# Performance work log

Measured on AMD Instinct MI355X. Metric: run time of the kernel, lower is better.

Reference implementation:

```python
import jax, jax.numpy as jnp
import numpy as np

K_UPPER = 196608  # number of smallest-|grad| positions to mask per sample


def setup_inputs() -> dict:
    key = jax.random.key(0)
    k1, k2 = jax.random.split(key)
    x = jax.random.normal(k1, (64, 3, 512, 512), dtype=jnp.float32)
    grad = jax.random.normal(k2, (64, 3, 512, 512), dtype=jnp.float32)
    return {"x": x, "grad": grad}


def _mask_low_gradient(x, grad):
    # x, grad: [B, C, H, W]
    B, C, H, W = x.shape
    hw = H * W
    flat_g = grad.reshape(B, -1)                                  # [B, C*H*W]
    # _sort: k smallest absolute gradients -> top_k of negated abs (unsorted ok)
    _neg_vals, idx = jax.lax.top_k(-jnp.abs(flat_g), K_UPPER)     # idx: [B, K]
    # channel containing each selected flat index (matches the torch range test)
    ch = idx // hw                                                # [B, K]
    xc = x.reshape(B, C, hw)
    # Faithful to source: torch slice [start:channel_indexes] EXCLUDES the last
    # element of each channel when computing min/max.
    mn = jnp.min(xc[:, :, : hw - 1], axis=-1)                     # [B, C]
    mx = jnp.max(xc[:, :, : hw - 1], axis=-1)                     # [B, C]
    lo = jnp.take_along_axis(mn, ch, axis=1)                      # [B, K]
    hi = jnp.take_along_axis(mx, ch, axis=1)                      # [B, K]
    # uniform fill in [lo, hi) per masked element
    u = jax.random.uniform(jax.random.key(42), idx.shape, dtype=x.dtype)
    fill = lo + u * (hi - lo)                                     # [B, K]
    flat_x = x.reshape(B, -1)
    out = flat_x.at[jnp.arange(B)[:, None], idx].set(fill)
    return out.reshape(x.shape)


def reference(x, grad):
    return _mask_low_gradient(x, grad)
```

## Files before the change

### kernel.cpp

```cpp
#include <hip/hip_runtime.h>
#include <stdint.h>

#define TPB 256
#define TPS 1024

constexpr int BN   = 64;
constexpr int CCH  = 3;
constexpr int HWS  = 262144;
constexpr int LOG_HW = 18;
constexpr int NPS  = 786432;
constexpr int KSEL = 196608;
constexpr int KCAP = 200704;
constexpr int NB_T = 32;
constexpr int CH_T = NPS / NB_T;
constexpr int NB_C = 64;
constexpr int CH_C = NPS / NB_C;
constexpr int NRNG = 768;
constexpr int NB_S = 8;
constexpr int CH_S = KCAP / NB_S;
constexpr int TILE = 4096;
constexpr int NBINS = 2048;
constexpr int SUB  = 8;
constexpr int NFB  = 49;
constexpr int ASLOT = 256;
constexpr int ACAP = NRNG * ASLOT;
constexpr int BMPW = NPS / 32;

typedef unsigned u32x4 __attribute__((ext_vector_type(4)));

constexpr int WS_MN   = 0;
constexpr int WS_MX   = 192;
constexpr int WS_V1   = 384;
constexpr int WS_B1   = 448;
constexpr int WS_V2   = 512;
constexpr int WS_GS   = 576;
constexpr int WS_KP   = 640;
constexpr int WS_S0   = 704;
constexpr int WS_S01  = 768;
constexpr int WS_CNT  = 832;
constexpr int WS_COFF = WS_CNT + BN * NRNG;
constexpr int WS_MNP  = WS_COFF + BN * NRNG;
constexpr int WS_MXP  = WS_MNP + BN * CCH * SUB;
constexpr int WS_CNT2 = WS_MXP + BN * CCH * SUB;
constexpr int WS_RC   = WS_CNT2 + BN * NRNG;
constexpr int WS_CHC  = WS_RC + BN * NRNG;
constexpr int WS_THA  = WS_CHC + BN * 4;
constexpr int WS_THB  = WS_THA + BN * NBINS;
constexpr int WS_H0   = WS_THB + BN * NBINS;
constexpr int WS_H1   = WS_H0 + BN * 256 * NB_S;
constexpr int WS_H2   = WS_H1 + BN * 256 * NB_S;
constexpr int WS_H3   = WS_H2 + BN * 256 * NB_S;
constexpr int WS_HF   = WS_H3 + BN * 256 * NB_S;
constexpr size_t WS_FIX_END = (size_t)WS_HF + (size_t)BN * 64 * NB_S;
constexpr size_t RECW = (size_t)BN * KCAP * 2;
constexpr size_t WS_NEEDED_BYTES = (WS_FIX_END + 2 * RECW) * 4;
constexpr size_t WS_BMP_OFF = WS_FIX_END + 2 * RECW;
constexpr size_t WS_NEEDED_BMP = (WS_BMP_OFF + (size_t)BN * BMPW) * 4;
static_assert((size_t)BN * ACAP <= RECW, "append scratch must fit in R2");

__device__ __forceinline__ unsigned rotl32(unsigned x, int r) { return (x << r) | (x >> (32 - r)); }

__device__ __forceinline__ void tf4(unsigned& x0, unsigned& x1, int a, int b, int c, int d) {
  x0 += x1; x1 = rotl32(x1, a); x1 ^= x0;
  x0 += x1; x1 = rotl32(x1, b); x1 ^= x0;
  x0 += x1; x1 = rotl32(x1, c); x1 ^= x0;
  x0 += x1; x1 = rotl32(x1, d); x1 ^= x0;
}

__device__ __forceinline__ void threefry2x32(unsigned k0, unsigned k1, unsigned c0, unsigned c1,
                                             unsigned& o0, unsigned& o1) {
  const unsigned ks2 = k0 ^ k1 ^ 0x1BD11BDAu;
  unsigned x0 = c0 + k0, x1 = c1 + k1;
  tf4(x0, x1, 13, 15, 26, 6);  x0 += k1;  x1 += ks2 + 1u;
  tf4(x0, x1, 17, 29, 16, 24); x0 += ks2; x1 += k0 + 2u;
  tf4(x0, x1, 13, 15, 26, 6);  x0 += k0;  x1 += k1 + 3u;
  tf4(x0, x1, 17, 29, 16, 24); x0 += k1;  x1 += ks2 + 4u;
  tf4(x0, x1, 13, 15, 26, 6);  x0 += ks2; x1 += k0 + 5u;
  o0 = x0; o1 = x1;
}

__global__ __launch_bounds__(TPB) void k_zero(unsigned* __restrict__ p, int n) {
  int i = blockIdx.x * TPB + threadIdx.x;
  if (i < n) p[i] = 0u;
}

__global__ __launch_bounds__(TPB) void k_mnmx(const float4* __restrict__ x,
                                              unsigned* __restrict__ ws) {
  __shared__ float smn[TPB], smx[TPB];
  const int g = blockIdx.x;
  const int bc = g / SUB, sub = g - bc * SUB;
  const int Q4 = HWS / 4 / SUB;
  const size_t base4 = (size_t)bc * (HWS / 4) + (size_t)sub * Q4;
  const bool last = (sub == SUB - 1);
  const int tid = threadIdx.x;
  float lo = 3.4e38f, hi = -3.4e38f;
  for (int i = tid; i < Q4; i += TPB) {
    float4 v = x[base4 + i];
    if (last && i == Q4 - 1) {
      lo = fminf(lo, fminf(fminf(v.x, v.y), v.z));
      hi = fmaxf(hi, fmaxf(fmaxf(v.x, v.y), v.z));
    } else {
      lo = fminf(lo, fminf(fminf(v.x, v.y), fminf(v.z, v.w)));
      hi = fmaxf(hi, fmaxf(fmaxf(v.x, v.y), fmaxf(v.z, v.w)));
    }
  }
  smn[tid] = lo; smx[tid] = hi; __syncthreads();
  for (int s = TPB / 2; s > 0; s >>= 1) {
    if (tid < s) { smn[tid] = fminf(smn[tid], smn[tid + s]); smx[tid] = fmaxf(smx[tid], smx[tid + s]); }
    __syncthreads();
  }
  if (tid == 0) {
    ((float*)(ws + WS_MNP))[g] = smn[0];
    ((float*)(ws + WS_MXP))[g] = smx[0];
  }
}

__global__ __launch_bounds__(TPB) void k_mnfin(unsigned* __restrict__ ws) {
  const int t = threadIdx.x;
  if (t < BN * CCH) {
    const float* mnp = (const float*)(ws + WS_MNP);
    const float* mxp = (const float*)(ws + WS_MXP);
    float lo = 3.4e38f, hi = -3.4e38f;
    for (int s = 0; s < SUB; ++s) {
      lo = fminf(lo, mnp[t * SUB + s]);
      hi = fmaxf(hi, mxp[t * SUB + s]);
    }
    ((float*)(ws + WS_MN))[t] = lo;
    ((float*)(ws + WS_MX))[t] = hi;
  }
}

__global__ __launch_bounds__(TPB) void k_thrA(const unsigned* __restrict__ gb, unsigned* __restrict__ hist) {
  __shared__ unsigned h[NBINS];
  const int b = blockIdx.y, blk = blockIdx.x, tid = threadIdx.x;
  for (int v = tid; v < NBINS; v += TPB) h[v] = 0u;
  __syncthreads();
  const uint4* g4 = (const uint4*)(gb + (size_t)b * NPS + (size_t)blk * CH_T);
  for (int i = tid; i < CH_T / 4; i += TPB) {
    uint4 v = g4[i];
    atomicAdd(&h[(v.x & 0x7FFFFFFFu) >> 21], 1u);
    atomicAdd(&h[(v.y & 0x7FFFFFFFu) >> 21], 1u);
    atomicAdd(&h[(v.z & 0x7FFFFFFFu) >> 21], 1u);
    atomicAdd(&h[(v.w & 0x7FFFFFFFu) >> 21], 1u);
  }
  __syncthreads();
  unsigned* gh = hist + (size_t)b * NBINS;
  for (int v = tid; v < NBINS; v += TPB) if (h[v]) atomicAdd(&gh[v], h[v]);
}

__global__ __launch_bounds__(TPB) void k_thrBC(const unsigned* __restrict__ gb,
                                               unsigned* __restrict__ hist,
                                               unsigned* __restrict__ app,
                                               unsigned* __restrict__ ws) {
  __shared__ unsigned h[NBINS];
  __shared__ unsigned chs[3];
  const int bid = blockIdx.x;
  const int b = bid & 63, blk = bid >> 6, tid = threadIdx.x;
  const int lane = tid & 63, wv = tid >> 6;
  const unsigned long long ltm = (1ull << lane) - 1ull;
  for (int v = tid; v < NBINS; v += TPB) h[v] = 0u;
  if (tid < 3) chs[tid] = 0u;
  __syncthreads();
  const unsigned V1 = ws[WS_V1 + b];
  const uint4* g4 = (const uint4*)(gb + (size_t)b * NPS + (size_t)blk * CH_C) + wv * 768;
  unsigned cc0 = 0, cc1 = 0, cc2 = 0;
  for (int r = 0; r < 3; ++r) {
    const unsigned rangeId = (unsigned)((blk * 4 + wv) * 3 + r);
    unsigned* ap = app + (size_t)b * ACAP + (size_t)rangeId * ASLOT;
    unsigned abase = 0, cntLess = 0;
#pragma unroll
    for (int it = 0; it < 4; ++it) {
      const uint4 v = g4[r * 256 + it * 64 + lane];
      const unsigned e = (unsigned)blk * CH_C + (unsigned)wv * 3072u + (unsigned)r * 1024u
                       + (unsigned)it * 256u + (unsigned)lane * 4u;
      const unsigned k[4] = { v.x & 0x7FFFFFFFu, v.y & 0x7FFFFFFFu, v.z & 0x7FFFFFFFu, v.w & 0x7FFFFFFFu };
#pragma unroll
      for (int c = 0; c < 4; ++c) {
        const unsigned top = k[c] >> 21;
        const bool isEq = (top == V1);
        if (top < V1) {
          ++cntLess;
          const unsigned ch = (e + (unsigned)c) >> LOG_HW;
          if (ch == 0) ++cc0; else if (ch == 1) ++cc1; else ++cc2;
        } else if (isEq) {
          atomicAdd(&h[(k[c] >> 10) & 2047u], 1u);
        }
        unsigned long long m = __ballot(isEq);
        if (isEq) {
          const unsigned ai = abase + (unsigned)__popcll(m & ltm);
          if (ai < (unsigned)ASLOT) {
            const unsigned ch = (e + (unsigned)c) >> LOG_HW;
            ap[ai] = (ch << 11) | ((k[c] >> 10) & 2047u);
          }
        }
        abase += (unsigned)__popcll(m);
      }
    }
    unsigned cl = cntLess;
    for (int off = 32; off >= 1; off >>= 1) cl += __shfl_down(cl, off, 64);
    if (lane == 0) {
      ws[WS_CNT + b * NRNG + rangeId] = cl;
      ws[WS_RC + b * NRNG + rangeId] = min(abase, (unsigned)ASLOT);
    }
  }
  if (cc0) atomicAdd(&chs[0], cc0);
  if (cc1) atomicAdd(&chs[1], cc1);
  if (cc2) atomicAdd(&chs[2], cc2);
  __syncthreads();
  if (tid < 3 && chs[tid]) atomicAdd(&ws[WS_CHC + b * 4 + tid], chs[tid]);
  unsigned* gh = hist + (size_t)b * NBINS;
  for (int v = tid; v < NBINS; v += TPB) if (h[v]) atomicAdd(&gh[v], h[v]);
}

__global__ __launch_bounds__(TPB) void k_find(const unsigned* __restrict__ hist,
                                              unsigned* __restrict__ ws, int mode) {
  __shared__ unsigned part[TPB];
  const int b = blockIdx.x, tid = threadIdx.x;
  const unsigned* h = hist + (size_t)b * NBINS;
  const int per = NBINS / TPB;
  const unsigned Kt = (mode == 0) ? (unsigned)KSEL : (unsigned)KSEL - ws[WS_B1 + b];
  unsigned vals[8];
  unsigned s = 0;
  for (int j = 0; j < per; ++j) { vals[j] = h[tid * per + j]; s += vals[j]; }
  part[tid] = s; __syncthreads();
  for (int off = 1; off < TPB; off <<= 1) {
    unsigned t = (tid >= off) ? part[tid - off] : 0u;
    __syncthreads(); part[tid] += t; __syncthreads();
  }
  unsigned run = part[tid] - s;
  for (int j = 0; j < per; ++j) {
    const unsigned lo = run, c = vals[j];
    run += c;
    if (lo < Kt && Kt <= run) {
      const unsigned v = (unsigned)(tid * per + j);
      if (mode == 0) {
        ws[WS_V1 + b] = v; ws[WS_B1 + b] = lo;
      } else {
        ws[WS_V2 + b] = v;
        const unsigned T22 = (ws[WS_V1 + b] << 11) | v;
        ws[WS_GS + b] = (T22 << 10) | 1023u;
        unsigned kp = ws[WS_B1 + b] + lo + c;
        if (kp > (unsigned)KCAP) kp = (unsigned)KCAP;
        ws[WS_KP + b] = kp;
      }
    }
  }
}

__global__ __launch_bounds__(TPB) void k_cc2(const unsigned* __restrict__ app,
                                             unsigned* __restrict__ ws) {
  __shared__ unsigned lch[3];
  const int b = blockIdx.x, tid = threadIdx.x;
  if (tid < 3) lch[tid] = 0u;
  __syncthreads();
  const unsigned V2 = ws[WS_V2 + b];
  unsigned c0 = 0, c1 = 0, c2 = 0;
  for (int j = 0; j < 3; ++j) {
    const int r = j * 256 + tid;
    const unsigned cnt = ws[WS_RC + b * NRNG + r];
    const unsigned* ap = app + (size_t)b * ACAP + (size_t)r * ASLOT;
    unsigned n2 = 0;
    for (unsigned i = 0; i < cnt; ++i) {
      const unsigned e = ap[i];
      if ((e & 2047u) <= V2) {
        ++n2;
        const unsigned ch = (e >> 11) & 3u;
        if (ch == 0) ++c0; else if (ch == 1) ++c1; else ++c2;
      }
    }
    ws[WS_CNT2 + b * NRNG + r] = n2;
  }
  if (c0) atomicAdd(&lch[0], c0);
  if (c1) atomicAdd(&lch[1], c1);
  if (c2) atomicAdd(&lch[2], c2);
  __syncthreads();
  if (tid < 3 && lch[tid]) atomicAdd(&ws[WS_CHC + b * 4 + tid], lch[tid]);
}

__global__ __launch_bounds__(TPB) void k_cscan(unsigned* __restrict__ ws) {
  __shared__ unsigned wsum[4];
  const int b = blockIdx.x, tid = threadIdx.x;
  const int lane = tid & 63, wv = tid >> 6;
  const unsigned c0 = ws[WS_CNT + b * NRNG + 3 * tid + 0] + ws[WS_CNT2 + b * NRNG + 3 * tid + 0];
  const unsigned c1 = ws[WS_CNT + b * NRNG + 3 * tid + 1] + ws[WS_CNT2 + b * NRNG + 3 * tid + 1];
  const unsigned c2 = ws[WS_CNT + b * NRNG + 3 * tid + 2] + ws[WS_CNT2 + b * NRNG + 3 * tid + 2];
  const unsigned s = c0 + c1 + c2;
  unsigned incl = s;
  for (int off = 1; off < 64; off <<= 1) {
    unsigned t = __shfl_up(incl, off, 64);
    if (lane >= off) incl += t;
  }
  if (lane == 63) wsum[wv] = incl;
  __syncthreads();
  unsigned wpre = 0;
  for (int w = 0; w < wv; ++w) wpre += wsum[w];
  const unsigned excl = incl - s + wpre;
  ws[WS_COFF + b * NRNG + 3 * tid + 0] = excl;
  ws[WS_COFF + b * NRNG + 3 * tid + 1] = excl + c0;
  ws[WS_COFF + b * NRNG + 3 * tid + 2] = excl + c0 + c1;
  if (tid == 0) {
    const unsigned s0 = ws[WS_CHC + b * 4 + 0];
    ws[WS_S0 + b] = s0;
    ws[WS_S01 + b] = s0 + ws[WS_CHC + b * 4 + 1];
  }
}

template<int BMP>
__global__ __launch_bounds__(TPB) void k_cscatter(const unsigned* __restrict__ gb,
                                                  const unsigned* __restrict__ ws,
                                                  unsigned* __restrict__ keyArr,
                                                  unsigned* __restrict__ H0,
                                                  unsigned* __restrict__ bmp) {
  __shared__ unsigned h2[256 * NB_S];
  const int bid = blockIdx.x;
  const int b = bid & 63, blk = bid >> 6, tid = threadIdx.x;
  const int lane = tid & 63, wv = tid >> 6;
  for (int e = tid; e < 256 * NB_S; e += TPB) h2[e] = 0u;
  __syncthreads();
  const unsigned G = ws[WS_GS + b];
  const uint4* g4 = (const uint4*)(gb + (size_t)b * NPS + (size_t)blk * CH_C) + wv * 768;
  unsigned* ka = keyArr + (size_t)b * KCAP;
  unsigned* bw = BMP ? (bmp + (size_t)b * BMPW + (size_t)blk * 384 + (size_t)wv * 96) : nullptr;
  for (int r = 0; r < 3; ++r) {
    unsigned base = ws[WS_COFF + b * NRNG + (blk * 4 + wv) * 3 + r];
#pragma unroll
    for (int it = 0; it < 4; ++it) {
      const uint4 v = g4[r * 256 + it * 64 + lane];
      unsigned k[4] = { v.x & 0x7FFFFFFFu, v.y & 0x7FFFFFFFu, v.z & 0x7FFFFFFFu, v.w & 0x7FFFFFFFu };
      unsigned nib = 0;
      unsigned cnt = 0;
      bool s[4];
#pragma unroll
      for (int c = 0; c < 4; ++c) {
        s[c] = (k[c] <= G);
        nib |= ((unsigned)s[c]) << c;
        cnt += (unsigned)s[c];
      }
      if (BMP) {
        unsigned w = nib << ((lane & 7) * 4);
        w |= __shfl_xor(w, 1, 64);
        w |= __shfl_xor(w, 2, 64);
        w |= __shfl_xor(w, 4, 64);
        if ((lane & 7) == 0) bw[r * 32 + it * 8 + (lane >> 3)] = w;
      }
      unsigned incl = cnt;
      for (int off = 1; off < 64; off <<= 1) {
        unsigned u = __shfl_up(incl, off, 64);
        if (lane >= off) incl += u;
      }
      const unsigned wtot = __shfl(incl, 63, 64);
      unsigned pos = base + incl - cnt;
#pragma unroll
      for (int c = 0; c < 4; ++c) {
        if (s[c]) {
          if (pos < (unsigned)KCAP) {
            ka[pos] = k[c];
            atomicAdd(&h2[(k[c] & 255u) * NB_S + pos / (unsigned)CH_S], 1u);
          }
          ++pos;
        }
      }
      base += wtot;
    }
  }
  __syncthreads();
  unsigned* Hb = H0 + (size_t)b * 256 * NB_S;
  for (int e = tid; e < 256 * NB_S; e += TPB) {
    unsigned c = h2[e];
    if (c) atomicAdd(&Hb[e], c);
  }
}

__global__ __launch_bounds__(TPB) void k_hscan(unsigned* __restrict__ H) {
  __shared__ unsigned wsum[4];
  const int b = blockIdx.x, tid = threadIdx.x;
  const int lane = tid & 63, wv = tid >> 6;
  unsigned* Hb = H + (size_t)b * 256 * NB_S;
  unsigned row[NB_S];
  unsigned run = 0;
#pragma unroll
  for (int k = 0; k < NB_S; ++k) {
    unsigned t = Hb[tid * NB_S + k];
    row[k] = run; run += t;
  }
  unsigned incl = run;
  for (int off = 1; off < 64; off <<= 1) {
    unsigned t = __shfl_up(incl, off, 64);
    if (lane >= off) incl += t;
  }
  if (lane == 63) wsum[wv] = incl;
  __syncthreads();
  unsigned wpre = 0;
  for (int w = 0; w < wv; ++w) wpre += wsum[w];
  const unsigned excl = incl - run + wpre;
#pragma unroll
  for (int k = 0; k < NB_S; ++k) Hb[tid * NB_S + k] = row[k] + excl;
}

__global__ __launch_bounds__(64) void k_hscanF(unsigned* __restrict__ Hf) {
  const int b = blockIdx.x, tid = threadIdx.x;
  unsigned* Hb = Hf + (size_t)b * 64 * NB_S;
  unsigned row[NB_S];
  unsigned run = 0;
  if (tid < NFB) {
#pragma unroll
    for (int k = 0; k < NB_S; ++k) {
      unsigned t = Hb[tid * NB_S + k];
      row[k] = run; run += t;
    }
  }
  unsigned incl = run;
  for (int off = 1; off < 64; off <<= 1) {
    unsigned t = __shfl_up(incl, off, 64);
    if (tid >= off) incl += t;
  }
  const unsigned excl = incl - run;
  if (tid < NFB) {
#pragma unroll
    for (int k = 0; k < NB_S; ++k) Hb[tid * NB_S + k] = row[k] + excl;
  }
}

template<int MODE>
__global__ __launch_bounds__(TPS) void k_sort8(const unsigned* __restrict__ keyIn,
                                               const uint2* __restrict__ inR,
                                               uint2* __restrict__ outR,
                                               const unsigned* __restrict__ Hcur,
                                               unsigned* __restrict__ Hnext,
                                               unsigned* __restrict__ Hf,
                                               const unsigned* __restrict__ ws,
                                               int shift) {
  __shared__ unsigned wh[16][256];
  __shared__ unsigned gout[256];
  __shared__ unsigned gbase[256];
  __shared__ unsigned wsum[4];
  __shared__ uint2    stg[TILE];
  __shared__ unsigned h2[256 * NB_S];
  __shared__ unsigned h2f[(MODE == 1) ? NFB * NB_S : 1];
  const int bid = blockIdx.x;
  const int b = bid & 63, blk = bid >> 6, tid = threadIdx.x;
  const int lane = tid & 63, wv = tid >> 6;
  const unsigned long long ltm = (1ull << lane) - 1ull;
  const unsigned kp = min(ws[WS_KP + b], (unsigned)KCAP);
  const unsigned s0 = (unsigned)blk * CH_S;
  const unsigned s1 = min(s0 + (unsigned)CH_S, kp);
  const unsigned* ki = keyIn + (size_t)b * KCAP;
  const uint2* in = inR + (size_t)b * KCAP;
  uint2* out = outR + (size_t)b * KCAP;
  const bool doF = (MODE == 1) && (Hf != nullptr);

  for (int d = tid; d < 256; d += TPS) gbase[d] = Hcur[((size_t)b * 256 + d) * NB_S + blk];
  for (int e = tid; e < 256 * NB_S; e += TPS) h2[e] = 0u;
  if (MODE == 1) { if (doF) for (int e = tid; e < NFB * NB_S; e += TPS) h2f[e] = 0u; }
  __syncthreads();

  for (unsigned t0 = s0; t0 < s1; t0 += (unsigned)TILE) {
    { uint4* w4 = (uint4*)&wh[0][0];
      w4[tid] = make_uint4(0u, 0u, 0u, 0u); }
    __syncthreads();

    unsigned key[4], cpp[4], wloc[4], dig[4];
    bool val[4];
    const unsigned wbase = t0 + (unsigned)wv * 256u;
#pragma unroll
    for (int c = 0; c < 4; ++c) {
      const unsigned i = wbase + (unsigned)c * 64u + (unsigned)lane;
      val[c] = (i < s1);
      if (MODE == 0) { cpp[c] = i; key[c] = val[c] ? ki[i] : 0u; }
      else { uint2 r = val[c] ? in[i] : make_uint2(0u, 0u); cpp[c] = r.x; key[c] = r.y; }
      dig[c] = (key[c] >> shift) & 255u;
      unsigned long long peers = __ballot(val[c]);
#pragma unroll
      for (int bit = 0; bit < 8; ++bit) {
        unsigned long long bb = __ballot(val[c] && ((dig[c] >> bit) & 1u));
        peers &= ((dig[c] >> bit) & 1u) ? bb : ~bb;
      }
      const unsigned before = (unsigned)__popcll(peers & ltm);
      int ldr = __ffsll((unsigned long long)peers) - 1;
      if (ldr < 0) ldr = 0;
      unsigned old = 0;
      if (val[c] && lane == ldr) old = atomicAdd(&wh[wv][dig[c]], (unsigned)__popcll(peers));
      old = __shfl(old, ldr, 64);
      wloc[c] = old + before;
    }
    __syncthreads();

    unsigned incl = 0, tot = 0;
    if (tid < 256) {
      const unsigned d = (unsigned)tid;
#pragma unroll
      for (int w = 0; w < 16; ++w) tot += wh[w][d];
      incl = tot;
      for (int off = 1; off < 64; off <<= 1) {
        unsigned t = __shfl_up(incl, off, 64);
        if (lane >= off) incl += t;
      }
      if (lane == 63) wsum[wv] = incl;
    }
    __syncthreads();
    if (tid < 256) {
      const unsigned d = (unsigned)tid;
      unsigned wpre = 0;
      for (int w = 0; w < wv; ++w) wpre += wsum[w];
      const unsigned tstart = incl - tot + wpre;
      const unsigned g = gbase[d];
      gout[d] = g - tstart;
      gbase[d] = g + tot;
      unsigned run = tstart;
#pragma unroll
      for (int w = 0; w < 16; ++w) { const unsigned t = wh[w][d]; wh[w][d] = run; run += t; }
    }
    __syncthreads();

#pragma unroll
    for (int c = 0; c < 4; ++c) {
      if (val[c]) {
        uint2 r; r.x = cpp[c]; r.y = key[c];
        stg[wh[wv][dig[c]] + wloc[c]] = r;
      }
    }
    __syncthreads();
    const unsigned nt = min((unsigned)TILE, s1 - t0);
    for (unsigned j = tid; j < nt; j += TPS) {
      const uint2 r = stg[j];
      const unsigned d = (r.y >> shift) & 255u;
      const unsigned pos = gout[d] + j;
      out[pos] = r;
      const unsigned nd = (r.y >> (shift + 8)) & 255u;
      atomicAdd(&h2[nd * NB_S + pos / (unsigned)CH_S], 1u);
      if (doF) atomicAdd(&h2f[(r.x >> 12) * NB_S + pos / (unsigned)CH_S], 1u);
    }
    __syncthreads();
  }

  {
    unsigned* Hb = Hnext + (size_t)b * 256 * NB_S;
    for (int e = tid; e < 256 * NB_S; e += TPS) {
      unsigned c = h2[e];
      if (c) atomicAdd(&Hb[e], c);
    }
    if (doF) {
      unsigned* Hfb = Hf + (size_t)b * 64 * NB_S;
      for (int e = tid; e < NFB * NB_S; e += TPS) {
        unsigned c = h2f[e];
        if (c) atomicAdd(&Hfb[e], c);
      }
    }
  }
}

__global__ __launch_bounds__(TPS) void k_final(const uint2* __restrict__ inR,
                                               uint2* __restrict__ pairOut,
                                               const unsigned* __restrict__ Hcur,
                                               const unsigned* __restrict__ Hf,
                                               const unsigned* __restrict__ ws) {
  __shared__ unsigned wh[16][128];
  __shared__ unsigned gbase[128];
  __shared__ unsigned whF[16][64];
  __shared__ unsigned goutF[64];
  __shared__ unsigned gbaseF[64];
  __shared__ uint2    stg[TILE];
  const int bid = blockIdx.x;
  const int b = bid & 63, blk = bid >> 6, tid = threadIdx.x;
  const int lane = tid & 63, wv = tid >> 6;
  const unsigned long long ltm = (1ull << lane) - 1ull;
  const unsigned kp = min(ws[WS_KP + b], (unsigned)KCAP);
  const unsigned s0 = (unsigned)blk * CH_S;
  const unsigned s1 = min(s0 + (unsigned)CH_S, kp);
  const uint2* in = inR + (size_t)b * KCAP;
  uint2* po = pairOut + (size_t)b * KCAP;

  for (int d = tid; d < 128; d += TPS) gbase[d] = Hcur[((size_t)b * 256 + d) * NB_S + blk];
  for (int d = tid; d < 64; d += TPS)
    gbaseF[d] = (d < NFB) ? Hf[((size_t)b * 64 + d) * NB_S + blk] : 0u;
  __syncthreads();

  for (unsigned t0 = s0; t0 < s1; t0 += (unsigned)TILE) {
    { uint4* p = (uint4*)&wh[0][0];
      if (tid < 512) p[tid] = make_uint4(0u, 0u, 0u, 0u);
      uint4* q = (uint4*)&whF[0][0];
      if (tid >= 512 && tid < 768) q[tid - 512] = make_uint4(0u, 0u, 0u, 0u); }
    __syncthreads();

    unsigned key[4], cpp[4], wloc[4], dig[4];
    bool val[4];
    const unsigned wbase = t0 + (unsigned)wv * 256u;
#pragma unroll
    for (int c = 0; c < 4; ++c) {
      const unsigned i = wbase + (unsigned)c * 64u + (unsigned)lane;
      val[c] = (i < s1);
      uint2 r = val[c] ? in[i] : make_uint2(0u, 0u);
      cpp[c] = r.x; key[c] = r.y;
      dig[c] = (key[c] >> 24) & 127u;
      unsigned long long peers = __ballot(val[c]);
#pragma unroll
      for (int bit = 0; bit < 7; ++bit) {
        unsigned long long bb = __ballot(val[c] && ((dig[c] >> bit) & 1u));
        peers &= ((dig[c] >> bit) & 1u) ? bb : ~bb;
      }
      const unsigned before = (unsigned)__popcll(peers & ltm);
      int ldr = __ffsll((unsigned long long)peers) - 1;
      if (ldr < 0) ldr = 0;
      unsigned old = 0;
      if (val[c] && lane == ldr) old = atomicAdd(&wh[wv][dig[c]], (unsigned)__popcll(peers));
      old = __shfl(old, ldr, 64);
      wloc[c] = old + before;
    }
    __syncthreads();

    if (tid < 128) {
      const unsigned d = (unsigned)tid;
      unsigned run = gbase[d];
#pragma unroll
      for (int w = 0; w < 16; ++w) { const unsigned t = wh[w][d]; wh[w][d] = run; run += t; }
      gbase[d] = run;
    }
    __syncthreads();

    unsigned rnk[4], dbF[4], wlocF[4];
#pragma unroll
    for (int c = 0; c < 4; ++c) {
      dbF[c] = cpp[c] >> 12;
      if (val[c]) {
        rnk[c] = wh[wv][dig[c]] + wloc[c];
        wlocF[c] = atomicAdd(&whF[wv][dbF[c]], 1u);
      }
    }
    __syncthreads();

    if (tid < 64) {
      const unsigned d = (unsigned)tid;
      unsigned tot = 0;
      if (d < NFB) {
#pragma unroll
        for (int w = 0; w < 16; ++w) tot += whF[w][d];
      }
      unsigned incl = tot;
      for (int off = 1; off < 64; off <<= 1) {
        unsigned t = __shfl_up(incl, off, 64);
        if (lane >= off) incl += t;
      }
      const unsigned tstart = incl - tot;
      goutF[d] = gbaseF[d] - tstart;
      gbaseF[d] += tot;
      unsigned run = tstart;
#pragma unroll
      for (int w = 0; w < 16; ++w) { const unsigned t = whF[w][d]; whF[w][d] = run; run += t; }
    }
    __syncthreads();

#pragma unroll
    for (int c = 0; c < 4; ++c) {
      if (val[c]) {
        uint2 r; r.x = cpp[c]; r.y = rnk[c];
        stg[whF[wv][dbF[c]] + wlocF[c]] = r;
      }
    }
    __syncthreads();

    const unsigned nt = min((unsigned)TILE, s1 - t0);
    for (unsigned j = tid; j < nt; j += TPS) {
      const uint2 r = stg[j];
      po[goutF[r.x >> 12] + j] = r;
    }
    __syncthreads();
  }
}

__global__ __launch_bounds__(TPB) void k_unpack(const uint2* __restrict__ pairs,
                                                unsigned* __restrict__ fm,
                                                const unsigned* __restrict__ ws) {
  __shared__ unsigned vals[4096];
  const int bid = blockIdx.x;
  const int b = bid & 63, d = bid >> 6, tid = threadIdx.x;
  const unsigned kp = min(ws[WS_KP + b], (unsigned)KCAP);
  const unsigned start = (unsigned)d * 4096u;
  if (start >= kp) return;
  const unsigned cnt = min(4096u, kp - start);
  const unsigned S0 = ws[WS_S0 + b], S01 = ws[WS_S01 + b];
  const float* mnf = (const float*)(ws + WS_MN);
  const float* mxf = (const float*)(ws + WS_MX);
  const float l0 = mnf[b * CCH], l1 = mnf[b * CCH + 1], l2 = mnf[b * CCH + 2];
  const float h0 = mxf[b * CCH], h1 = mxf[b * CCH + 1], h2v = mxf[b * CCH + 2];
  const uint2* pb = pairs + (size_t)b * KCAP + start;
  for (unsigned j = tid; j < cnt; j += TPB) {
    const uint2 r = pb[j];
    unsigned res = 0xFFFFFFFFu;
    if (r.y < (unsigned)KSEL) {
      const unsigned p = (unsigned)b * (unsigned)KSEL + r.y;
      unsigned o0, o1;
      threefry2x32(0u, 42u, 0u, p, o0, o1);
      const unsigned bits = o0 ^ o1;
      const float u = __uint_as_float((bits >> 9) | 0x3f800000u) - 1.0f;
      const unsigned ch = (unsigned)(r.x >= S0) + (unsigned)(r.x >= S01);
      const float lo = (ch == 0) ? l0 : ((ch == 1) ? l1 : l2);
      const float hi = (ch == 0) ? h0 : ((ch == 1) ? h1 : h2v);
      res = __float_as_uint(lo + u * (hi - lo));
    }
    vals[r.x & 4095u] = res;
  }
  __syncthreads();
  unsigned* f = fm + (size_t)b * KCAP + start;
  for (unsigned j = tid; j < cnt; j += TPB) f[j] = vals[j];
}

template<int BMP>
__global__ __launch_bounds__(TPB) void k_fill(const u32x4* __restrict__ x4,
                                              const u32x4* __restrict__ g4all,
                                              const unsigned* __restrict__ bmp,
                                              const unsigned* __restrict__ fillmap,
                                              const unsigned* __restrict__ ws,
                                              u32x4* __restrict__ out4) {
  const int bid = blockIdx.x;
  const int b = bid & 63, blk = bid >> 6, tid = threadIdx.x;
  const int lane = tid & 63, wv = tid >> 6;
  const unsigned G = ws[WS_GS + b];
  const unsigned kp = min(ws[WS_KP + b], (unsigned)KCAP);
  const size_t t4 = (size_t)b * (NPS / 4) + (size_t)blk * (CH_C / 4) + (size_t)wv * 768;
  const unsigned* fm = fillmap + (size_t)b * KCAP;
  const unsigned* bw = BMP ? (bmp + (size_t)b * BMPW + (size_t)blk * 384 + (size_t)wv * 96) : nullptr;
  for (int r = 0; r < 3; ++r) {
    unsigned base = ws[WS_COFF + b * NRNG + (blk * 4 + wv) * 3 + r];
#pragma unroll
    for (int it = 0; it < 4; ++it) {
      const size_t a = t4 + r * 256 + it * 64 + lane;
      u32x4 xv = __builtin_nontemporal_load(&x4[a]);
      unsigned nib;
      if (BMP) {
        const unsigned w = bw[r * 32 + it * 8 + (lane >> 3)];
        nib = (w >> ((lane & 7) * 4)) & 0xFu;
      } else {
        const u32x4 gv = __builtin_nontemporal_load(&g4all[a]);
        nib = (unsigned)((gv.x & 0x7FFFFFFFu) <= G)
            | ((unsigned)((gv.y & 0x7FFFFFFFu) <= G) << 1)
            | ((unsigned)((gv.z & 0x7FFFFFFFu) <= G) << 2)
            | ((unsigned)((gv.w & 0x7FFFFFFFu) <= G) << 3);
      }
      const unsigned cnt = (unsigned)__popc(nib);
      unsigned incl = cnt;
      for (int off = 1; off < 64; off <<= 1) {
        unsigned u = __shfl_up(incl, off, 64);
        if (lane >= off) incl += u;
      }
      const unsigned wtot = __shfl(incl, 63, 64);
      unsigned pos = base + incl - cnt;
#pragma unroll
      for (int c = 0; c < 4; ++c) {
        if ((nib >> c) & 1u) {
          if (pos < kp) {
            const unsigned rr = fm[pos];
            if (rr != 0xFFFFFFFFu) xv[c] = rr;
          }
          ++pos;
        }
      }
      __builtin_nontemporal_store(xv, &out4[a]);
      base += wtot;
    }
  }
}

extern "C" void kernel_launch(void* const* d_in, const int* in_sizes, int n_in,
                              void* d_out, int out_size, void* d_ws, size_t ws_size,
                              hipStream_t stream) {
  const float* x = (const float*)d_in[0];
  const unsigned* gb = (const unsigned*)d_in[1];
  float* out = (float*)d_out;
  unsigned* ws = (unsigned*)d_ws;
  if (ws_size < WS_NEEDED_BYTES) return;
  const bool useBmp = (ws_size >= WS_NEEDED_BMP);

  unsigned* R1 = ws + WS_FIX_END;
  unsigned* R2 = ws + WS_FIX_END + RECW;
  unsigned* BMP = ws + WS_BMP_OFF;
  unsigned* H0 = ws + WS_H0;
  unsigned* H1 = ws + WS_H1;
  unsigned* H2 = ws + WS_H2;
  unsigned* H3 = ws + WS_H3;
  unsigned* HF = ws + WS_HF;

  dim3 blk(TPB);
  dim3 sblk(TPS);

  k_mnmx<<<dim3(BN * CCH * SUB), blk, 0, stream>>>((const float4*)x, ws);
  k_mnfin<<<dim3(1), blk, 0, stream>>>(ws);
  {
    const int nz = (int)(WS_FIX_END - WS_CHC);
    k_zero<<<dim3((nz + TPB - 1) / TPB), blk, 0, stream>>>(ws + WS_CHC, nz);
  }

  k_thrA<<<dim3(NB_T, BN), blk, 0, stream>>>(gb, ws + WS_THA);
  k_find<<<dim3(BN), blk, 0, stream>>>(ws + WS_THA, ws, 0);
  k_thrBC<<<dim3(NB_C * BN), blk, 0, stream>>>(gb, ws + WS_THB, R2, ws);
  k_find<<<dim3(BN), blk, 0, stream>>>(ws + WS_THB, ws, 1);
  k_cc2<<<dim3(BN), blk, 0, stream>>>(R2, ws);
  k_cscan<<<dim3(BN), blk, 0, stream>>>(ws);

  if (useBmp) k_cscatter<1><<<dim3(NB_C * BN), blk, 0, stream>>>(gb, ws, R1, H0, BMP);
  else        k_cscatter<0><<<dim3(NB_C * BN), blk, 0, stream>>>(gb, ws, R1, H0, nullptr);

  k_hscan<<<dim3(BN), blk, 0, stream>>>(H0);
  k_sort8<0><<<dim3(NB_S * BN), sblk, 0, stream>>>(R1, (const uint2*)nullptr, (uint2*)R2, H0, H1, nullptr, ws, 0);
  k_hscan<<<dim3(BN), blk, 0, stream>>>(H1);
  k_sort8<1><<<dim3(NB_S * BN), sblk, 0, stream>>>(nullptr, (const uint2*)R2, (uint2*)R1, H1, H2, nullptr, ws, 8);
  k_hscan<<<dim3(BN), blk, 0, stream>>>(H2);
  k_sort8<1><<<dim3(NB_S * BN), sblk, 0, stream>>>(nullptr, (const uint2*)R1, (uint2*)R2, H2, H3, HF, ws, 16);
  k_hscan<<<dim3(BN), blk, 0, stream>>>(H3);
  k_hscanF<<<dim3(BN), dim3(64), 0, stream>>>(HF);

  k_final<<<dim3(NB_S * BN), sblk, 0, stream>>>((const uint2*)R2, (uint2*)R1, H3, HF, ws);
  k_unpack<<<dim3(NFB * BN), blk, 0, stream>>>((const uint2*)R1, R2, ws);

  if (useBmp) k_fill<1><<<dim3(NB_C * BN), blk, 0, stream>>>((const u32x4*)x, nullptr, BMP, R2, ws, (u32x4*)out);
  else        k_fill<0><<<dim3(NB_C * BN), blk, 0, stream>>>((const u32x4*)x, (const u32x4*)gb, nullptr, R2, ws, (u32x4*)out);
}
```

Measured before the change: 708.5 us.

## Use per-wave-iteration ranges with ballot-popcount offsets instead of shuffle scans

Splits each sample into 3072 ranges instead of 768, so every 256-element wave iteration gets its own precomputed output offset. The compaction kernels then compute lane positions with four ballots plus popcounts instead of a 6-step shuffle prefix scan. Less-than counts and append counts are packed into one word, which removes the separate CNT2/RC arrays. The shared-histogram clearing in the sort passes moves to the end of each tile so one barrier per tile goes away. The cost is a larger offset array and scan work, and append slots shrink to 64 per range, which could overflow on skewed inputs.

```diff
diff --git a/kernel.cpp b/kernel.cpp
--- a/kernel.cpp
+++ b/kernel.cpp
@@ -15,14 +15,14 @@
 constexpr int CH_T = NPS / NB_T;
 constexpr int NB_C = 64;
 constexpr int CH_C = NPS / NB_C;
-constexpr int NRNG = 768;
+constexpr int NRNG = 3072;
 constexpr int NB_S = 8;
 constexpr int CH_S = KCAP / NB_S;
 constexpr int TILE = 4096;
 constexpr int NBINS = 2048;
 constexpr int SUB  = 8;
 constexpr int NFB  = 49;
-constexpr int ASLOT = 256;
+constexpr int ASLOT = 64;
 constexpr int ACAP = NRNG * ASLOT;
 constexpr int BMPW = NPS / 32;
 
@@ -41,9 +41,7 @@
 constexpr int WS_COFF = WS_CNT + BN * NRNG;
 constexpr int WS_MNP  = WS_COFF + BN * NRNG;
 constexpr int WS_MXP  = WS_MNP + BN * CCH * SUB;
-constexpr int WS_CNT2 = WS_MXP + BN * CCH * SUB;
-constexpr int WS_RC   = WS_CNT2 + BN * NRNG;
-constexpr int WS_CHC  = WS_RC + BN * NRNG;
+constexpr int WS_CHC  = WS_MXP + BN * CCH * SUB;
 constexpr int WS_THA  = WS_CHC + BN * 4;
 constexpr int WS_THB  = WS_THA + BN * NBINS;
 constexpr int WS_H0   = WS_THB + BN * NBINS;
@@ -163,49 +161,55 @@
   __syncthreads();
   const unsigned V1 = ws[WS_V1 + b];
   const uint4* g4 = (const uint4*)(gb + (size_t)b * NPS + (size_t)blk * CH_C) + wv * 768;
-  unsigned cc0 = 0, cc1 = 0, cc2 = 0;
-  for (int r = 0; r < 3; ++r) {
-    const unsigned rangeId = (unsigned)((blk * 4 + wv) * 3 + r);
+  unsigned cc0 = 0, cc1 = 0, cc2v = 0;
+  for (int it = 0; it < 12; ++it) {
+    const unsigned rangeId = (unsigned)((blk * 4 + wv) * 12 + it);
     unsigned* ap = app + (size_t)b * ACAP + (size_t)rangeId * ASLOT;
-    unsigned abase = 0, cntLess = 0;
-#pragma unroll
-    for (int it = 0; it < 4; ++it) {
-      const uint4 v = g4[r * 256 + it * 64 + lane];
-      const unsigned e = (unsigned)blk * CH_C + (unsigned)wv * 3072u + (unsigned)r * 1024u
-                       + (unsigned)it * 256u + (unsigned)lane * 4u;
-      const unsigned k[4] = { v.x & 0x7FFFFFFFu, v.y & 0x7FFFFFFFu, v.z & 0x7FFFFFFFu, v.w & 0x7FFFFFFFu };
-#pragma unroll
-      for (int c = 0; c < 4; ++c) {
-        const unsigned top = k[c] >> 21;
-        const bool isEq = (top == V1);
-        if (top < V1) {
-          ++cntLess;
+    const uint4 v = g4[it * 64 + lane];
+    const unsigned e = (unsigned)blk * CH_C + (unsigned)wv * 3072u + (unsigned)it * 256u
+                     + (unsigned)lane * 4u;
+    const unsigned k[4] = { v.x & 0x7FFFFFFFu, v.y & 0x7FFFFFFFu, v.z & 0x7FFFFFFFu, v.w & 0x7FFFFFFFu };
+    unsigned nibL = 0, nibE = 0;
+#pragma unroll
+    for (int c = 0; c < 4; ++c) {
+      const unsigned top = k[c] >> 21;
+      if (top < V1) {
+        nibL |= 1u << c;
+        const unsigned ch = (e + (unsigned)c) >> LOG_HW;
+        if (ch == 0) ++cc0; else if (ch == 1) ++cc1; else ++cc2v;
+      } else if (top == V1) {
+        nibE |= 1u << c;
+        atomicAdd(&h[(k[c] >> 10) & 2047u], 1u);
+      }
+    }
+    unsigned long long mL[4], mE[4];
+#pragma unroll
+    for (int c = 0; c < 4; ++c) {
+      mL[c] = __ballot((nibL >> c) & 1u);
+      mE[c] = __ballot((nibE >> c) & 1u);
+    }
+    const unsigned lanePreE = (unsigned)__popcll(mE[0] & ltm) + (unsigned)__popcll(mE[1] & ltm)
+                            + (unsigned)__popcll(mE[2] & ltm) + (unsigned)__popcll(mE[3] & ltm);
+    const unsigned totE = (unsigned)__popcll(mE[0]) + (unsigned)__popcll(mE[1])
+                        + (unsigned)__popcll(mE[2]) + (unsigned)__popcll(mE[3]);
+    const unsigned cl = (unsigned)__popcll(mL[0]) + (unsigned)__popcll(mL[1])
+                      + (unsigned)__popcll(mL[2]) + (unsigned)__popcll(mL[3]);
+#pragma unroll
+    for (int c = 0; c < 4; ++c) {
+      if ((nibE >> c) & 1u) {
+        const unsigned ai = lanePreE + (unsigned)__popc(nibE & ((1u << c) - 1u));
+        if (ai < (unsigned)ASLOT) {
           const unsigned ch = (e + (unsigned)c) >> LOG_HW;
-          if (ch == 0) ++cc0; else if (ch == 1) ++cc1; else ++cc2;
-        } else if (isEq) {
-          atomicAdd(&h[(k[c] >> 10) & 2047u], 1u);
+          ap[ai] = (ch << 11) | ((k[c] >> 10) & 2047u);
         }
-        unsigned long long m = __ballot(isEq);
-        if (isEq) {
-          const unsigned ai = abase + (unsigned)__popcll(m & ltm);
-          if (ai < (unsigned)ASLOT) {
-            const unsigned ch = (e + (unsigned)c) >> LOG_HW;
-            ap[ai] = (ch << 11) | ((k[c] >> 10) & 2047u);
-          }
-        }
-        abase += (unsigned)__popcll(m);
-      }
-    }
-    unsigned cl = cntLess;
-    for (int off = 32; off >= 1; off >>= 1) cl += __shfl_down(cl, off, 64);
-    if (lane == 0) {
-      ws[WS_CNT + b * NRNG + rangeId] = cl;
-      ws[WS_RC + b * NRNG + rangeId] = min(abase, (unsigned)ASLOT);
-    }
+      }
+    }
+    if (lane == 0)
+      ws[WS_CNT + b * NRNG + rangeId] = cl | (min(totE, (unsigned)ASLOT) << 16);
   }
   if (cc0) atomicAdd(&chs[0], cc0);
   if (cc1) atomicAdd(&chs[1], cc1);
-  if (cc2) atomicAdd(&chs[2], cc2);
+  if (cc2v) atomicAdd(&chs[2], cc2v);
   __syncthreads();
   if (tid < 3 && chs[tid]) atomicAdd(&ws[WS_CHC + b * 4 + tid], chs[tid]);
   unsigned* gh = hist + (size_t)b * NBINS;
@@ -255,12 +259,13 @@
   __syncthreads();
   const unsigned V2 = ws[WS_V2 + b];
   unsigned c0 = 0, c1 = 0, c2 = 0;
-  for (int j = 0; j < 3; ++j) {
-    const int r = j * 256 + tid;
-    const unsigned cnt = ws[WS_RC + b * NRNG + r];
+  for (int j = 0; j < 12; ++j) {
+    const int r = tid * 12 + j;
+    const unsigned w = ws[WS_CNT + b * NRNG + r];
+    const unsigned rc = w >> 16;
     const unsigned* ap = app + (size_t)b * ACAP + (size_t)r * ASLOT;
     unsigned n2 = 0;
-    for (unsigned i = 0; i < cnt; ++i) {
+    for (unsigned i = 0; i < rc; ++i) {
       const unsigned e = ap[i];
       if ((e & 2047u) <= V2) {
         ++n2;
@@ -268,7 +273,7 @@
         if (ch == 0) ++c0; else if (ch == 1) ++c1; else ++c2;
       }
     }
-    ws[WS_CNT2 + b * NRNG + r] = n2;
+    ws[WS_CNT + b * NRNG + r] = w + n2;
   }
   if (c0) atomicAdd(&lch[0], c0);
   if (c1) atomicAdd(&lch[1], c1);
@@ -281,10 +286,13 @@
   __shared__ unsigned wsum[4];
   const int b = blockIdx.x, tid = threadIdx.x;
   const int lane = tid & 63, wv = tid >> 6;
-  const unsigned c0 = ws[WS_CNT + b * NRNG + 3 * tid + 0] + ws[WS_CNT2 + b * NRNG + 3 * tid + 0];
-  const unsigned c1 = ws[WS_CNT + b * NRNG + 3 * tid + 1] + ws[WS_CNT2 + b * NRNG + 3 * tid + 1];
-  const unsigned c2 = ws[WS_CNT + b * NRNG + 3 * tid + 2] + ws[WS_CNT2 + b * NRNG + 3 * tid + 2];
-  const unsigned s = c0 + c1 + c2;
+  unsigned loc[12];
+  unsigned s = 0;
+#pragma unroll
+  for (int j = 0; j < 12; ++j) {
+    const unsigned t = ws[WS_CNT + b * NRNG + tid * 12 + j] & 0xFFFFu;
+    loc[j] = s; s += t;
+  }
   unsigned incl = s;
   for (int off = 1; off < 64; off <<= 1) {
     unsigned t = __shfl_up(incl, off, 64);
@@ -295,9 +303,8 @@
   unsigned wpre = 0;
   for (int w = 0; w < wv; ++w) wpre += wsum[w];
   const unsigned excl = incl - s + wpre;
-  ws[WS_COFF + b * NRNG + 3 * tid + 0] = excl;
-  ws[WS_COFF + b * NRNG + 3 * tid + 1] = excl + c0;
-  ws[WS_COFF + b * NRNG + 3 * tid + 2] = excl + c0 + c1;
+#pragma unroll
+  for (int j = 0; j < 12; ++j) ws[WS_COFF + b * NRNG + tid * 12 + j] = excl + loc[j];
   if (tid == 0) {
     const unsigned s0 = ws[WS_CHC + b * 4 + 0];
     ws[WS_S0 + b] = s0;
@@ -315,52 +322,41 @@
   const int bid = blockIdx.x;
   const int b = bid & 63, blk = bid >> 6, tid = threadIdx.x;
   const int lane = tid & 63, wv = tid >> 6;
+  const unsigned long long ltm = (1ull << lane) - 1ull;
   for (int e = tid; e < 256 * NB_S; e += TPB) h2[e] = 0u;
   __syncthreads();
   const unsigned G = ws[WS_GS + b];
   const uint4* g4 = (const uint4*)(gb + (size_t)b * NPS + (size_t)blk * CH_C) + wv * 768;
   unsigned* ka = keyArr + (size_t)b * KCAP;
   unsigned* bw = BMP ? (bmp + (size_t)b * BMPW + (size_t)blk * 384 + (size_t)wv * 96) : nullptr;
-  for (int r = 0; r < 3; ++r) {
-    unsigned base = ws[WS_COFF + b * NRNG + (blk * 4 + wv) * 3 + r];
-#pragma unroll
-    for (int it = 0; it < 4; ++it) {
-      const uint4 v = g4[r * 256 + it * 64 + lane];
-      unsigned k[4] = { v.x & 0x7FFFFFFFu, v.y & 0x7FFFFFFFu, v.z & 0x7FFFFFFFu, v.w & 0x7FFFFFFFu };
-      unsigned nib = 0;
-      unsigned cnt = 0;
-      bool s[4];
-#pragma unroll
-      for (int c = 0; c < 4; ++c) {
-        s[c] = (k[c] <= G);
-        nib |= ((unsigned)s[c]) << c;
-        cnt += (unsigned)s[c];
-      }
-      if (BMP) {
-        unsigned w = nib << ((lane & 7) * 4);
-        w |= __shfl_xor(w, 1, 64);
-        w |= __shfl_xor(w, 2, 64);
-        w |= __shfl_xor(w, 4, 64);
-        if ((lane & 7) == 0) bw[r * 32 + it * 8 + (lane >> 3)] = w;
-      }
-      unsigned incl = cnt;
-      for (int off = 1; off < 64; off <<= 1) {
-        unsigned u = __shfl_up(incl, off, 64);
-        if (lane >= off) incl += u;
-      }
-      const unsigned wtot = __shfl(incl, 63, 64);
-      unsigned pos = base + incl - cnt;
-#pragma unroll
-      for (int c = 0; c < 4; ++c) {
-        if (s[c]) {
-          if (pos < (unsigned)KCAP) {
-            ka[pos] = k[c];
-            atomicAdd(&h2[(k[c] & 255u) * NB_S + pos / (unsigned)CH_S], 1u);
-          }
-          ++pos;
+  for (int it = 0; it < 12; ++it) {
+    const unsigned off = ws[WS_COFF + b * NRNG + (blk * 4 + wv) * 12 + it];
+    const uint4 v = g4[it * 64 + lane];
+    unsigned k[4] = { v.x & 0x7FFFFFFFu, v.y & 0x7FFFFFFFu, v.z & 0x7FFFFFFFu, v.w & 0x7FFFFFFFu };
+    unsigned nib = 0;
+#pragma unroll
+    for (int c = 0; c < 4; ++c) nib |= ((unsigned)(k[c] <= G)) << c;
+    if (BMP) {
+      unsigned w = nib << ((lane & 7) * 4);
+      w |= __shfl_xor(w, 1, 64);
+      w |= __shfl_xor(w, 2, 64);
+      w |= __shfl_xor(w, 4, 64);
+      if ((lane & 7) == 0) bw[it * 8 + (lane >> 3)] = w;
+    }
+    unsigned long long m[4];
+#pragma unroll
+    for (int c = 0; c < 4; ++c) m[c] = __ballot((nib >> c) & 1u);
+    const unsigned lanePre = (unsigned)__popcll(m[0] & ltm) + (unsigned)__popcll(m[1] & ltm)
+                           + (unsigned)__popcll(m[2] & ltm) + (unsigned)__popcll(m[3] & ltm);
+#pragma unroll
+    for (int c = 0; c < 4; ++c) {
+      if ((nib >> c) & 1u) {
+        const unsigned pos = off + lanePre + (unsigned)__popc(nib & ((1u << c) - 1u));
+        if (pos < (unsigned)KCAP) {
+          ka[pos] = k[c];
+          atomicAdd(&h2[(k[c] & 255u) * NB_S + pos / (unsigned)CH_S], 1u);
         }
       }
-      base += wtot;
     }
   }
   __syncthreads();
@@ -452,13 +448,10 @@
   for (int d = tid; d < 256; d += TPS) gbase[d] = Hcur[((size_t)b * 256 + d) * NB_S + blk];
   for (int e = tid; e < 256 * NB_S; e += TPS) h2[e] = 0u;
   if (MODE == 1) { if (doF) for (int e = tid; e < NFB * NB_S; e += TPS) h2f[e] = 0u; }
+  { uint4* w4 = (uint4*)&wh[0][0]; w4[tid] = make_uint4(0u, 0u, 0u, 0u); }
   __syncthreads();
 
   for (unsigned t0 = s0; t0 < s1; t0 += (unsigned)TILE) {
-    { uint4* w4 = (uint4*)&wh[0][0];
-      w4[tid] = make_uint4(0u, 0u, 0u, 0u); }
-    __syncthreads();
-
     unsigned key[4], cpp[4], wloc[4], dig[4];
     bool val[4];
     const unsigned wbase = t0 + (unsigned)wv * 256u;
@@ -530,6 +523,7 @@
       atomicAdd(&h2[nd * NB_S + pos / (unsigned)CH_S], 1u);
       if (doF) atomicAdd(&h2f[(r.x >> 12) * NB_S + pos / (unsigned)CH_S], 1u);
     }
+    { uint4* w4 = (uint4*)&wh[0][0]; w4[tid] = make_uint4(0u, 0u, 0u, 0u); }
     __syncthreads();
   }
 
@@ -573,15 +567,13 @@
   for (int d = tid; d < 128; d += TPS) gbase[d] = Hcur[((size_t)b * 256 + d) * NB_S + blk];
   for (int d = tid; d < 64; d += TPS)
     gbaseF[d] = (d < NFB) ? Hf[((size_t)b * 64 + d) * NB_S + blk] : 0u;
+  { uint4* p = (uint4*)&wh[0][0];
+    if (tid < 512) p[tid] = make_uint4(0u, 0u, 0u, 0u);
+    uint4* q = (uint4*)&whF[0][0];
+    if (tid >= 512 && tid < 768) q[tid - 512] = make_uint4(0u, 0u, 0u, 0u); }
   __syncthreads();
 
   for (unsigned t0 = s0; t0 < s1; t0 += (unsigned)TILE) {
-    { uint4* p = (uint4*)&wh[0][0];
-      if (tid < 512) p[tid] = make_uint4(0u, 0u, 0u, 0u);
-      uint4* q = (uint4*)&whF[0][0];
-      if (tid >= 512 && tid < 768) q[tid - 512] = make_uint4(0u, 0u, 0u, 0u); }
-    __syncthreads();
-
     unsigned key[4], cpp[4], wloc[4], dig[4];
     bool val[4];
     const unsigned wbase = t0 + (unsigned)wv * 256u;
@@ -663,6 +655,10 @@
       const uint2 r = stg[j];
       po[goutF[r.x >> 12] + j] = r;
     }
+    { uint4* p = (uint4*)&wh[0][0];
+      if (tid < 512) p[tid] = make_uint4(0u, 0u, 0u, 0u);
+      uint4* q = (uint4*)&whF[0][0];
+      if (tid >= 512 && tid < 768) q[tid - 512] = make_uint4(0u, 0u, 0u, 0u); }
     __syncthreads();
   }
 }
@@ -717,46 +713,40 @@
   const unsigned G = ws[WS_GS + b];
   const unsigned kp = min(ws[WS_KP + b], (unsigned)KCAP);
   const size_t t4 = (size_t)b * (NPS / 4) + (size_t)blk * (CH_C / 4) + (size_t)wv * 768;
+  const unsigned long long ltm = (1ull << lane) - 1ull;
   const unsigned* fm = fillmap + (size_t)b * KCAP;
   const unsigned* bw = BMP ? (bmp + (size_t)b * BMPW + (size_t)blk * 384 + (size_t)wv * 96) : nullptr;
-  for (int r = 0; r < 3; ++r) {
-    unsigned base = ws[WS_COFF + b * NRNG + (blk * 4 + wv) * 3 + r];
-#pragma unroll
-    for (int it = 0; it < 4; ++it) {
-      const size_t a = t4 + r * 256 + it * 64 + lane;
-      u32x4 xv = __builtin_nontemporal_load(&x4[a]);
-      unsigned nib;
-      if (BMP) {
-        const unsigned w = bw[r * 32 + it * 8 + (lane >> 3)];
-        nib = (w >> ((lane & 7) * 4)) & 0xFu;
-      } else {
-        const u32x4 gv = __builtin_nontemporal_load(&g4all[a]);
-        nib = (unsigned)((gv.x & 0x7FFFFFFFu) <= G)
-            | ((unsigned)((gv.y & 0x7FFFFFFFu) <= G) << 1)
-            | ((unsigned)((gv.z & 0x7FFFFFFFu) <= G) << 2)
-            | ((unsigned)((gv.w & 0x7FFFFFFFu) <= G) << 3);
-      }
-      const unsigned cnt = (unsigned)__popc(nib);
-      unsigned incl = cnt;
-      for (int off = 1; off < 64; off <<= 1) {
-        unsigned u = __shfl_up(incl, off, 64);
-        if (lane >= off) incl += u;
-      }
-      const unsigned wtot = __shfl(incl, 63, 64);
-      unsigned pos = base + incl - cnt;
-#pragma unroll
-      for (int c = 0; c < 4; ++c) {
-        if ((nib >> c) & 1u) {
-          if (pos < kp) {
-            const unsigned rr = fm[pos];
-            if (rr != 0xFFFFFFFFu) xv[c] = rr;
-          }
-          ++pos;
+  for (int it = 0; it < 12; ++it) {
+    const unsigned off = ws[WS_COFF + b * NRNG + (blk * 4 + wv) * 12 + it];
+    const size_t a = t4 + it * 64 + lane;
+    u32x4 xv = __builtin_nontemporal_load(&x4[a]);
+    unsigned nib;
+    if (BMP) {
+      const unsigned w = bw[it * 8 + (lane >> 3)];
+      nib = (w >> ((lane & 7) * 4)) & 0xFu;
+    } else {
+      const u32x4 gv = __builtin_nontemporal_load(&g4all[a]);
+      nib = (unsigned)((gv.x & 0x7FFFFFFFu) <= G)
+          | ((unsigned)((gv.y & 0x7FFFFFFFu) <= G) << 1)
+          | ((unsigned)((gv.z & 0x7FFFFFFFu) <= G) << 2)
+          | ((unsigned)((gv.w & 0x7FFFFFFFu) <= G) << 3);
+    }
+    unsigned long long m[4];
+#pragma unroll
+    for (int c = 0; c < 4; ++c) m[c] = __ballot((nib >> c) & 1u);
+    const unsigned lanePre = (unsigned)__popcll(m[0] & ltm) + (unsigned)__popcll(m[1] & ltm)
+                           + (unsigned)__popcll(m[2] & ltm) + (unsigned)__popcll(m[3] & ltm);
+#pragma unroll
+    for (int c = 0; c < 4; ++c) {
+      if ((nib >> c) & 1u) {
+        const unsigned pos = off + lanePre + (unsigned)__popc(nib & ((1u << c) - 1u));
+        if (pos < kp) {
+          const unsigned rr = fm[pos];
+          if (rr != 0xFFFFFFFFu) xv[c] = rr;
         }
       }
-      __builtin_nontemporal_store(xv, &out4[a]);
-      base += wtot;
-    }
+    }
+    __builtin_nontemporal_store(xv, &out4[a]);
   }
 }
 
```

Result: slower. 753.2 us (median of 4 runs) (+6.3%).
